# Performance work log

Hardware: AMD Instinct MI355X
Metric: run time of the kernel (lower is better)

Reference implementation:

```python
import jax, jax.numpy as jnp
import numpy as np

EMBED_DIM = 256
CPB_HIDDEN = 256
NUM_HEADS = 8
HEAD_DIM = EMBED_DIM // NUM_HEADS


def setup_inputs() -> dict:
    key = jax.random.key(0)
    ks = jax.random.split(key, 16)
    B, Q, K, D = 2, 256, 2048, EMBED_DIM
    s = 0.02
    return {
        "entities": jax.random.normal(ks[0], (B, Q, D), jnp.float32),
        "images": jax.random.normal(ks[1], (B, K, D), jnp.float32),
        "relative_distances": jax.random.normal(ks[2], (B, Q, K, 2), jnp.float32),
        "Wq": jax.random.normal(ks[3], (D, D), jnp.float32) * s,
        "bq": jnp.zeros((D,), jnp.float32),
        "Wkv": jax.random.normal(ks[4], (2 * D, D), jnp.float32) * s,
        "bkv": jnp.zeros((2 * D,), jnp.float32),
        "W1": jax.random.normal(ks[5], (CPB_HIDDEN, 2), jnp.float32) * s,
        "b1": jnp.zeros((CPB_HIDDEN,), jnp.float32),
        "W2": jax.random.normal(ks[6], (NUM_HEADS, CPB_HIDDEN), jnp.float32) * s,
        "b2": jnp.zeros((NUM_HEADS,), jnp.float32),
        "Wo": jax.random.normal(ks[7], (D, D), jnp.float32) * s,
        "bo": jnp.zeros((D,), jnp.float32),
    }


def reference(entities, images, relative_distances, Wq, bq, Wkv, bkv, W1, b1, W2, b2, Wo, bo):
    B, Q, D = entities.shape
    K = images.shape[1]
    H, hd = NUM_HEADS, HEAD_DIM
    # projections
    q = (entities @ Wq.T + bq).reshape(B, Q, H, hd).transpose(0, 2, 1, 3)  # B H Q hd
    kv = (images @ Wkv.T + bkv).reshape(B, K, 2, H, hd)
    k = kv[:, :, 0].transpose(0, 2, 1, 3)  # B H K hd
    v = kv[:, :, 1].transpose(0, 2, 1, 3)  # B H K hd
    # attention logits
    logits = jnp.einsum("bhqd,bhkd->bhqk", q, k) * (hd ** -0.5)
    # continuous position bias MLP: 2 -> hidden -> num_heads
    h = jax.nn.relu(relative_distances @ W1.T + b1)  # B Q K hidden
    cpb = h @ W2.T + b2  # B Q K H
    logits = logits + cpb.transpose(0, 3, 1, 2)
    attn = jax.nn.softmax(logits, axis=-1)
    out = jnp.einsum("bhqk,bhkd->bhqd", attn, v)
    out = out.transpose(0, 2, 1, 3).reshape(B, Q, D)
    return out @ Wo.T + bo
```

## Files before the change

kernel.cpp:

```cpp
#include <hip/hip_runtime.h>
#include <hip/hip_bf16.h>
#include <cstdint>
#include <cstddef>

#define B_  2
#define Q_  256
#define KL  2048
#define D_  256
#define H_  8
#define HD_ 32
#define CH_ 256

typedef _Float16 f16;
typedef __fp16 fp16x2 __attribute__((ext_vector_type(2)));
typedef _Float16 f16x8 __attribute__((ext_vector_type(8)));
typedef unsigned short ushortv4 __attribute__((ext_vector_type(4)));
typedef unsigned int uintv4 __attribute__((ext_vector_type(4)));
typedef float f32x4 __attribute__((ext_vector_type(4)));

union UH  { fp16x2 h; unsigned int u; };
union UH8 { f16x8 h; unsigned int u[4]; };

__device__ __forceinline__ unsigned int pkrtz(float a, float b) {
  UH r; r.h = __builtin_amdgcn_cvt_pkrtz(a, b); return r.u;
}
__device__ __forceinline__ unsigned short f16bits(float a) {
  return (unsigned short)(pkrtz(a, 0.f) & 0xffffu);
}
__device__ __forceinline__ unsigned int pk_fma(unsigned int a, unsigned int b,
                                               unsigned int c) {
  unsigned int d;
  asm("v_pk_fma_f16 %0, %1, %2, %3" : "=v"(d) : "v"(a), "v"(b), "v"(c));
  return d;
}
__device__ __forceinline__ unsigned int pk_max0(unsigned int a) {
  unsigned int d;
  asm("v_pk_max_f16 %0, %1, %2" : "=v"(d) : "v"(a), "v"(0u));
  return d;
}

__global__ __launch_bounds__(512) void prep(
    const float* __restrict__ ent, const float* __restrict__ img,
    const float* __restrict__ Wq, const float* __restrict__ Wkv,
    const float* __restrict__ Wo,
    unsigned short* __restrict__ entS, unsigned short* __restrict__ imgS,
    unsigned short* __restrict__ WqS, unsigned short* __restrict__ WkvS,
    unsigned short* __restrict__ WoS) {
  int bid = blockIdx.x, t = threadIdx.x;
  const float* src;
  unsigned short* dst;
  if (bid < 32)       { src = ent + (size_t)bid * 16 * D_;          dst = entS + (size_t)bid * 4096; }
  else if (bid < 288) { int k = bid - 32;  src = img + (size_t)k * 16 * D_; dst = imgS + (size_t)k * 4096; }
  else if (bid < 304) { int k = bid - 288; src = Wq  + (size_t)k * 16 * D_; dst = WqS  + (size_t)k * 4096; }
  else if (bid < 336) { int k = bid - 304; src = Wkv + (size_t)k * 16 * D_; dst = WkvS + (size_t)k * 4096; }
  else                { int k = bid - 336; src = Wo  + (size_t)k * 16 * D_; dst = WoS  + (size_t)k * 4096; }
  __shared__ float rows[16][257];
  {
    int rr = t >> 5, c0 = (t & 31) * 8;
    float4 a = *(const float4*)(src + rr * D_ + c0);
    float4 b = *(const float4*)(src + rr * D_ + c0 + 4);
    rows[rr][c0 + 0] = a.x; rows[rr][c0 + 1] = a.y;
    rows[rr][c0 + 2] = a.z; rows[rr][c0 + 3] = a.w;
    rows[rr][c0 + 4] = b.x; rows[rr][c0 + 5] = b.y;
    rows[rr][c0 + 6] = b.z; rows[rr][c0 + 7] = b.w;
  }
  __syncthreads();
  int s = t >> 6, l = t & 63, r = l & 15, g = l >> 4;
  const float* rp = &rows[r][s * 32 + g * 8];
  UH8 u;
#pragma unroll
  for (int m = 0; m < 4; ++m) u.u[m] = pkrtz(rp[2 * m], rp[2 * m + 1]);
  ((f16x8*)dst)[s * 64 + l] = u.h;
}

__global__ __launch_bounds__(256) void gemm2(
    const unsigned short* __restrict__ entS, const unsigned short* __restrict__ WqS,
    const float* __restrict__ bq, float* __restrict__ qp,
    const unsigned short* __restrict__ imgS, const unsigned short* __restrict__ WkvS,
    const float* __restrict__ bkv, unsigned short* __restrict__ kps,
    unsigned short* __restrict__ vt) {
  int bid = blockIdx.x;
  int t = threadIdx.x, w = t >> 6, l = t & 63;
  int r = l & 15, g = l >> 4;
  if (bid < 64) {
    int nt = bid & 3, mg = bid >> 2;
    const f16x8* A = (const f16x8*)entS;
    const f16x8* Bf = (const f16x8*)WqS;
    int tA0 = mg * 2, tB = nt * 4 + w;
    f16x8 a0[8], a1[8], bf[8];
#pragma unroll
    for (int s = 0; s < 8; ++s) {
      a0[s] = A[(tA0 * 8 + s) * 64 + l];
      a1[s] = A[((tA0 + 1) * 8 + s) * 64 + l];
      bf[s] = Bf[(tB * 8 + s) * 64 + l];
    }
    f32x4 acc0 = {0.f, 0.f, 0.f, 0.f}, acc1 = {0.f, 0.f, 0.f, 0.f};
#pragma unroll
    for (int s = 0; s < 8; ++s) {
      acc0 = __builtin_amdgcn_mfma_f32_16x16x32_f16(a0[s], bf[s], acc0, 0, 0, 0);
      acc1 = __builtin_amdgcn_mfma_f32_16x16x32_f16(a1[s], bf[s], acc1, 0, 0, 0);
    }
    int n = nt * 64 + w * 16 + r;
    float bb = bq[n];
    int m0 = mg * 32;
#pragma unroll
    for (int rr = 0; rr < 4; ++rr) {
      qp[(size_t)(m0 + g * 4 + rr) * D_ + n] = acc0[rr] + bb;
      qp[(size_t)(m0 + 16 + g * 4 + rr) * D_ + n] = acc1[rr] + bb;
    }
  } else {
    int bid2 = bid - 64;
    int nt = bid2 & 7, mg = (bid2 >> 3) & 63, b = bid2 >> 9;
    const f16x8* A = (const f16x8*)imgS;
    const f16x8* Bf = (const f16x8*)WkvS;
    int tA0 = b * 128 + mg * 2, tB = nt * 4 + w;
    f16x8 a0[8], a1[8], bf[8];
#pragma unroll
    for (int s = 0; s < 8; ++s) {
      a0[s] = A[(tA0 * 8 + s) * 64 + l];
      a1[s] = A[((tA0 + 1) * 8 + s) * 64 + l];
      bf[s] = Bf[(tB * 8 + s) * 64 + l];
    }
    f32x4 acc0 = {0.f, 0.f, 0.f, 0.f}, acc1 = {0.f, 0.f, 0.f, 0.f};
#pragma unroll
    for (int s = 0; s < 8; ++s) {
      acc0 = __builtin_amdgcn_mfma_f32_16x16x32_f16(a0[s], bf[s], acc0, 0, 0, 0);
      acc1 = __builtin_amdgcn_mfma_f32_16x16x32_f16(a1[s], bf[s], acc1, 0, 0, 0);
    }
    int n = nt * 64 + w * 16 + r;
    float bb = bkv[n];
#pragma unroll
    for (int mi = 0; mi < 2; ++mi) {
      f32x4 ac = (mi == 0) ? acc0 : acc1;
      int mt = mg * 2 + mi;
      if (n < 256) {
        int s2 = n >> 5, gg = (n >> 3) & 3, e = n & 7;
        size_t base = ((size_t)((b * 128 + mt) * 8 + s2) * 64 + gg * 16) * 8 + e;
#pragma unroll
        for (int rr = 0; rr < 4; ++rr)
          kps[base + (size_t)(g * 4 + rr) * 8] = f16bits(ac[rr] + bb);
      } else {
        int c = n - 256, h = c >> 5, dd = c & 31;
        ushortv4 p;
#pragma unroll
        for (int rr = 0; rr < 4; ++rr) p[rr] = f16bits(ac[rr] + bb);
        *(ushortv4*)(vt + ((size_t)(b * H_ + h) * HD_ + dd) * KL + mt * 16 + g * 4) = p;
      }
    }
  }
}

__global__ __launch_bounds__(256, 8) void logits_cpb(
    const float* __restrict__ qp, const unsigned short* __restrict__ kps,
    const float* __restrict__ rd, const float* __restrict__ W1,
    const float* __restrict__ b1, const float* __restrict__ W2,
    const float* __restrict__ b2, unsigned short* __restrict__ lgb,
    float* __restrict__ stats) {
  int gid = blockIdx.x;
  int kcg = gid & 15, qg = (gid >> 4) & 127, b = gid >> 11;
  int t = threadIdx.x;
  __shared__ unsigned int w1xs[128], w1ys[128], b1ps[128];
  __shared__ unsigned short w2h[H_][264];
  __shared__ unsigned int qs[2][128];
  __shared__ float b2s[H_];
  if (t < 128) {
    float4 wr = *(const float4*)(W1 + 4 * t);
    w1xs[t] = pkrtz(wr.x, wr.z);
    w1ys[t] = pkrtz(wr.y, wr.w);
    float2 bb = *(const float2*)(b1 + 2 * t);
    b1ps[t] = pkrtz(bb.x, bb.y);
  }
#pragma unroll
  for (int i = 0; i < 2; ++i) {
    int idx = t + i * 256;
    int h = idx >> 6, c0 = (idx & 63) * 4;
    float4 wv = *(const float4*)(W2 + h * CH_ + c0);
    w2h[h][c0 + 0] = f16bits(wv.x);
    w2h[h][c0 + 1] = f16bits(wv.y);
    w2h[h][c0 + 2] = f16bits(wv.z);
    w2h[h][c0 + 3] = f16bits(wv.w);
  }
  const float scale = 0.17677669529663687f;
  {
    int q = t >> 7, j = t & 127;
    float2 v = *(const float2*)(qp + ((size_t)(b * Q_ + qg * 2 + q) * D_) + 2 * j);
    qs[q][j] = pkrtz(v.x * scale, v.y * scale);
  }
  if (t < 8) b2s[t] = b2[t];
  __syncthreads();

  int l = t & 63, w = t >> 6;
  int hp = l & 15, g = l >> 4, hq = hp & 7;
  int k0 = kcg * 128 + w * 32;
  int kt0 = k0 >> 4;
  int cc = kcg * 4 + w;

  unsigned int x2[2][2], y2[2][2];
#pragma unroll
  for (int q = 0; q < 2; ++q) {
    const float* rdb = rd + ((size_t)(b * Q_ + qg * 2 + q) * KL) * 2;
#pragma unroll
    for (int r = 0; r < 2; ++r) {
      float2 p = *(const float2*)(rdb + (k0 + r * 16 + hp) * 2);
      x2[q][r] = pkrtz(p.x, p.x);
      y2[q][r] = pkrtz(p.y, p.y);
    }
  }

  f32x4 acc[2][2];
#pragma unroll
  for (int q = 0; q < 2; ++q)
#pragma unroll
    for (int r = 0; r < 2; ++r) acc[q][r] = (f32x4){0.f, 0.f, 0.f, 0.f};

  const f16x8* kb = (const f16x8*)kps + ((size_t)(b * 128 + kt0) * 8) * 64 + l;

#pragma unroll
  for (int s = 0; s < 8; ++s) {
    f16x8 kf[2];
#pragma unroll
    for (int r = 0; r < 2; ++r) kf[r] = kb[(r * 8 + s) * 64];
    int pidx = g * 4 + 16 * s;
    uintv4 wx = *(const uintv4*)&w1xs[pidx];
    uintv4 wy = *(const uintv4*)&w1ys[pidx];
    uintv4 bp = *(const uintv4*)&b1ps[pidx];
    f16x8 w2f = *(const f16x8*)&w2h[hq][g * 8 + 32 * s];
    bool sel = (hp == s);
#pragma unroll
    for (int q = 0; q < 2; ++q) {
      uintv4 qv = *(const uintv4*)&qs[q][s * 16 + g * 4];
      UH8 bq;
#pragma unroll
      for (int m = 0; m < 4; ++m) bq.u[m] = sel ? qv[m] : 0u;
#pragma unroll
      for (int r = 0; r < 2; ++r) {
        UH8 az;
#pragma unroll
        for (int m = 0; m < 4; ++m)
          az.u[m] = pk_max0(pk_fma(x2[q][r], wx[m], pk_fma(y2[q][r], wy[m], bp[m])));
        acc[q][r] = __builtin_amdgcn_mfma_f32_16x16x32_f16(az.h, w2f, acc[q][r], 0, 0, 0);
        acc[q][r] = __builtin_amdgcn_mfma_f32_16x16x32_f16(kf[r], bq.h, acc[q][r], 0, 0, 0);
      }
    }
  }

  float bhv = b2s[hq];
#pragma unroll
  for (int q = 0; q < 2; ++q) {
    int qrow = qg * 2 + q;
    float mx = -3.0e38f;
#pragma unroll
    for (int r = 0; r < 2; ++r)
#pragma unroll
      for (int rr = 0; rr < 4; ++rr) {
        acc[q][r][rr] += bhv;
        mx = fmaxf(mx, acc[q][r][rr]);
      }
    mx = fmaxf(mx, __shfl_xor(mx, 16));
    mx = fmaxf(mx, __shfl_xor(mx, 32));
    float ss = 0.f;
#pragma unroll
    for (int r = 0; r < 2; ++r)
#pragma unroll
      for (int rr = 0; rr < 4; ++rr) ss += __expf(acc[q][r][rr] - mx);
    ss += __shfl_xor(ss, 16);
    ss += __shfl_xor(ss, 32);
    if (l < 8)
      *(float2*)(stats + (((size_t)(b * H_ + l) * Q_ + qrow) * 64 + cc) * 2) =
          make_float2(mx, ss);
    if (hp < 8) {
      unsigned short* ob = lgb + ((size_t)(b * H_ + hp) * Q_ + qrow) * KL + k0;
#pragma unroll
      for (int r = 0; r < 2; ++r) {
        uint2 pk;
        pk.x = pkrtz(acc[q][r][0], acc[q][r][1]);
        pk.y = pkrtz(acc[q][r][2], acc[q][r][3]);
        *(uint2*)(ob + r * 16 + g * 4) = pk;
      }
    }
  }
}

__global__ __launch_bounds__(512) void sm_pv(const unsigned short* __restrict__ lgb,
                                             const float* __restrict__ stats,
                                             const unsigned short* __restrict__ vt,
                                             unsigned short* __restrict__ ctxb) {
  int gid = blockIdx.x;
  int qt = gid & 15, bh = gid >> 4;
  int t = threadIdx.x;
  __shared__ float Ms[16], Ss[16];
  __shared__ float pacc[8][16][33];

  {
    int row = t >> 5, cc = t & 31;
    const float2* sp = (const float2*)stats + ((size_t)bh * Q_ + qt * 16 + row) * 64;
    float2 s0 = sp[cc], s1 = sp[cc + 32];
    float m = fmaxf(s0.x, s1.x);
#pragma unroll
    for (int off = 16; off > 0; off >>= 1) m = fmaxf(m, __shfl_xor(m, off));
    float e = s0.y * __expf(s0.x - m) + s1.y * __expf(s1.x - m);
#pragma unroll
    for (int off = 16; off > 0; off >>= 1) e += __shfl_xor(e, off);
    if (cc == 0) { Ms[row] = m; Ss[row] = 1.0f / e; }
  }
  __syncthreads();

  int l = t & 63, w = t >> 6;
  int qq = l & 15, g = l >> 4;
  float mq = Ms[qq];
  const unsigned short* lr2 =
      lgb + ((size_t)bh * Q_ + qt * 16 + qq) * KL + w * 256 + g * 8;
  const unsigned short* vb0 =
      vt + ((size_t)bh * HD_ + qq) * KL + w * 256 + g * 8;
  const unsigned short* vb1 = vb0 + (size_t)16 * KL;
  f32x4 a0 = {0.f, 0.f, 0.f, 0.f}, a1 = {0.f, 0.f, 0.f, 0.f};
#pragma unroll
  for (int step = 0; step < 8; ++step) {
    f16x8 raw = *(const f16x8*)(lr2 + step * 32);
    UH8 pa;
#pragma unroll
    for (int mI = 0; mI < 4; ++mI) {
      float p0 = __expf((float)raw[2 * mI] - mq);
      float p1 = __expf((float)raw[2 * mI + 1] - mq);
      pa.u[mI] = pkrtz(p0, p1);
    }
    f16x8 v0 = *(const f16x8*)(vb0 + step * 32);
    f16x8 v1 = *(const f16x8*)(vb1 + step * 32);
    a0 = __builtin_amdgcn_mfma_f32_16x16x32_f16(pa.h, v0, a0, 0, 0, 0);
    a1 = __builtin_amdgcn_mfma_f32_16x16x32_f16(pa.h, v1, a1, 0, 0, 0);
  }
#pragma unroll
  for (int rr = 0; rr < 4; ++rr) {
    pacc[w][g * 4 + rr][qq] = a0[rr];
    pacc[w][g * 4 + rr][qq + 16] = a1[rr];
  }
  __syncthreads();

  {
    int qo = t >> 5, dd = t & 31;
    float sum = 0.f;
#pragma unroll
    for (int wv = 0; wv < 8; ++wv) sum += pacc[wv][qo][dd];
    sum *= Ss[qo];
    int b = bh >> 3, h = bh & 7;
    ctxb[((size_t)b * Q_ + qt * 16 + qo) * D_ + h * HD_ + dd] = f16bits(sum);
  }
}

__global__ __launch_bounds__(256) void gemm_o(const unsigned short* __restrict__ A,
                                              const unsigned short* __restrict__ WoS,
                                              const float* __restrict__ bias,
                                              float* __restrict__ out) {
  int nt = blockIdx.x & 3, mt = blockIdx.x >> 2;
  int t = threadIdx.x, w = t >> 6, l = t & 63;
  int m0 = mt * 16;
  int r = l & 15, g = l >> 4;
  const unsigned short* arow = A + (size_t)(m0 + r) * D_;
  int tB = nt * 4 + w;
  f16x8 af[8], bf[8];
#pragma unroll
  for (int s = 0; s < 8; ++s) {
    af[s] = *(const f16x8*)(arow + s * 32 + g * 8);
    bf[s] = ((const f16x8*)WoS)[(tB * 8 + s) * 64 + l];
  }
  f32x4 acc = {0.f, 0.f, 0.f, 0.f};
#pragma unroll
  for (int s = 0; s < 8; ++s)
    acc = __builtin_amdgcn_mfma_f32_16x16x32_f16(af[s], bf[s], acc, 0, 0, 0);
  int n = nt * 64 + w * 16 + r;
  float bb = bias[n];
#pragma unroll
  for (int rr = 0; rr < 4; ++rr)
    out[(size_t)(m0 + g * 4 + rr) * D_ + n] = acc[rr] + bb;
}

extern "C" void kernel_launch(void* const* d_in, const int* in_sizes, int n_in,
                              void* d_out, int out_size, void* d_ws, size_t ws_size,
                              hipStream_t stream) {
  const float* ent  = (const float*)d_in[0];
  const float* img  = (const float*)d_in[1];
  const float* rd   = (const float*)d_in[2];
  const float* Wq   = (const float*)d_in[3];
  const float* bq   = (const float*)d_in[4];
  const float* Wkv  = (const float*)d_in[5];
  const float* bkv  = (const float*)d_in[6];
  const float* W1   = (const float*)d_in[7];
  const float* b1   = (const float*)d_in[8];
  const float* W2   = (const float*)d_in[9];
  const float* b2   = (const float*)d_in[10];
  const float* Wo   = (const float*)d_in[11];
  const float* bo   = (const float*)d_in[12];
  float* out = (float*)d_out;

  char* ws = (char*)d_ws;
  float*          qp    = (float*)(ws + 0);
  unsigned short* kps   = (unsigned short*)(ws + 524288);
  unsigned short* vt    = (unsigned short*)(ws + 2621440);
  unsigned short* lgb   = (unsigned short*)(ws + 4718592);
  float*          stats = (float*)(ws + 21495808);
  unsigned short* ctxb  = (unsigned short*)(ws + 23592960);
  unsigned short* entS  = (unsigned short*)(ws + 23855104);
  unsigned short* imgS  = (unsigned short*)(ws + 24117248);
  unsigned short* WqS   = (unsigned short*)(ws + 26214400);
  unsigned short* WkvS  = (unsigned short*)(ws + 26345472);
  unsigned short* WoS   = (unsigned short*)(ws + 26607616);

  prep<<<dim3(352), dim3(512), 0, stream>>>(ent, img, Wq, Wkv, Wo,
                                            entS, imgS, WqS, WkvS, WoS);
  gemm2<<<dim3(64 + 1024), dim3(256), 0, stream>>>(entS, WqS, bq, qp,
                                                   imgS, WkvS, bkv, kps, vt);
  logits_cpb<<<dim3(B_ * 128 * 16), dim3(256), 0, stream>>>(qp, kps, rd, W1, b1, W2, b2, lgb, stats);
  sm_pv<<<dim3(B_ * H_ * 16), dim3(512), 0, stream>>>(lgb, stats, vt, ctxb);
  gemm_o<<<dim3(128), dim3(256), 0, stream>>>(ctxb, WoS, bo, out);
}
```

Measured before the change: 60.59 us.

## Store locally-normalized exp in logits kernel, rescale with packed multiply in PV

The logits kernel now writes exp(logit - chunk_max) in fp16 instead of raw logits. The PV kernel then rescales each 32-key chunk by exp(chunk_max - global_max), using a packed fp16 multiply, rather than recomputing eight exps per step. It also preloads all K fragments up front and relaxes launch bounds from 8 to 4 waves per SIMD to make room for the extra registers. This moves the exp work into the producer and removes it from the consumer's inner loop, at the cost of higher register pressure and lower occupancy.

After: 61.33 us. Within noise of the previous version (+1.2%).

```diff
diff --git a/kernel.cpp b/kernel.cpp
--- a/kernel.cpp
+++ b/kernel.cpp
@@ -36,6 +36,11 @@
 __device__ __forceinline__ unsigned int pk_max0(unsigned int a) {
   unsigned int d;
   asm("v_pk_max_f16 %0, %1, %2" : "=v"(d) : "v"(a), "v"(0u));
+  return d;
+}
+__device__ __forceinline__ unsigned int pk_mul(unsigned int a, unsigned int b) {
+  unsigned int d;
+  asm("v_pk_mul_f16 %0, %1, %2" : "=v"(d) : "v"(a), "v"(b));
   return d;
 }
 
@@ -150,7 +155,7 @@
   }
 }
 
-__global__ __launch_bounds__(256, 8) void logits_cpb(
+__global__ __launch_bounds__(256, 4) void logits_cpb(
     const float* __restrict__ qp, const unsigned short* __restrict__ kps,
     const float* __restrict__ rd, const float* __restrict__ W1,
     const float* __restrict__ b1, const float* __restrict__ W2,
@@ -195,6 +200,13 @@
   int kt0 = k0 >> 4;
   int cc = kcg * 4 + w;
 
+  const f16x8* kb = (const f16x8*)kps + ((size_t)(b * 128 + kt0) * 8) * 64 + l;
+  f16x8 kf[2][8];
+#pragma unroll
+  for (int r = 0; r < 2; ++r)
+#pragma unroll
+    for (int s = 0; s < 8; ++s) kf[r][s] = kb[(r * 8 + s) * 64];
+
   unsigned int x2[2][2], y2[2][2];
 #pragma unroll
   for (int q = 0; q < 2; ++q) {
@@ -213,13 +225,8 @@
 #pragma unroll
     for (int r = 0; r < 2; ++r) acc[q][r] = (f32x4){0.f, 0.f, 0.f, 0.f};
 
-  const f16x8* kb = (const f16x8*)kps + ((size_t)(b * 128 + kt0) * 8) * 64 + l;
-
 #pragma unroll
   for (int s = 0; s < 8; ++s) {
-    f16x8 kf[2];
-#pragma unroll
-    for (int r = 0; r < 2; ++r) kf[r] = kb[(r * 8 + s) * 64];
     int pidx = g * 4 + 16 * s;
     uintv4 wx = *(const uintv4*)&w1xs[pidx];
     uintv4 wy = *(const uintv4*)&w1ys[pidx];
@@ -239,7 +246,7 @@
         for (int m = 0; m < 4; ++m)
           az.u[m] = pk_max0(pk_fma(x2[q][r], wx[m], pk_fma(y2[q][r], wy[m], bp[m])));
         acc[q][r] = __builtin_amdgcn_mfma_f32_16x16x32_f16(az.h, w2f, acc[q][r], 0, 0, 0);
-        acc[q][r] = __builtin_amdgcn_mfma_f32_16x16x32_f16(kf[r], bq.h, acc[q][r], 0, 0, 0);
+        acc[q][r] = __builtin_amdgcn_mfma_f32_16x16x32_f16(kf[r][s], bq.h, acc[q][r], 0, 0, 0);
       }
     }
   }
@@ -258,11 +265,15 @@
       }
     mx = fmaxf(mx, __shfl_xor(mx, 16));
     mx = fmaxf(mx, __shfl_xor(mx, 32));
+    float ex[2][4];
     float ss = 0.f;
 #pragma unroll
     for (int r = 0; r < 2; ++r)
 #pragma unroll
-      for (int rr = 0; rr < 4; ++rr) ss += __expf(acc[q][r][rr] - mx);
+      for (int rr = 0; rr < 4; ++rr) {
+        ex[r][rr] = __expf(acc[q][r][rr] - mx);
+        ss += ex[r][rr];
+      }
     ss += __shfl_xor(ss, 16);
     ss += __shfl_xor(ss, 32);
     if (l < 8)
@@ -273,8 +284,8 @@
 #pragma unroll
       for (int r = 0; r < 2; ++r) {
         uint2 pk;
-        pk.x = pkrtz(acc[q][r][0], acc[q][r][1]);
-        pk.y = pkrtz(acc[q][r][2], acc[q][r][3]);
+        pk.x = pkrtz(ex[r][0], ex[r][1]);
+        pk.y = pkrtz(ex[r][2], ex[r][3]);
         *(uint2*)(ob + r * 16 + g * 4) = pk;
       }
     }
@@ -288,7 +299,8 @@
   int gid = blockIdx.x;
   int qt = gid & 15, bh = gid >> 4;
   int t = threadIdx.x;
-  __shared__ float Ms[16], Ss[16];
+  __shared__ float Ss[16];
+  __shared__ float scl[16][65];
   __shared__ float pacc[8][16][33];
 
   {
@@ -298,16 +310,18 @@
     float m = fmaxf(s0.x, s1.x);
 #pragma unroll
     for (int off = 16; off > 0; off >>= 1) m = fmaxf(m, __shfl_xor(m, off));
-    float e = s0.y * __expf(s0.x - m) + s1.y * __expf(s1.x - m);
+    float c0 = __expf(s0.x - m), c1 = __expf(s1.x - m);
+    float e = s0.y * c0 + s1.y * c1;
 #pragma unroll
     for (int off = 16; off > 0; off >>= 1) e += __shfl_xor(e, off);
-    if (cc == 0) { Ms[row] = m; Ss[row] = 1.0f / e; }
+    scl[row][cc] = c0;
+    scl[row][cc + 32] = c1;
+    if (cc == 0) Ss[row] = 1.0f / e;
   }
   __syncthreads();
 
   int l = t & 63, w = t >> 6;
   int qq = l & 15, g = l >> 4;
-  float mq = Ms[qq];
   const unsigned short* lr2 =
       lgb + ((size_t)bh * Q_ + qt * 16 + qq) * KL + w * 256 + g * 8;
   const unsigned short* vb0 =
@@ -316,14 +330,12 @@
   f32x4 a0 = {0.f, 0.f, 0.f, 0.f}, a1 = {0.f, 0.f, 0.f, 0.f};
 #pragma unroll
   for (int step = 0; step < 8; ++step) {
-    f16x8 raw = *(const f16x8*)(lr2 + step * 32);
+    UH8 raw = *(const UH8*)(lr2 + step * 32);
+    float sc = scl[qq][w * 8 + step];
+    unsigned int sc2 = pkrtz(sc, sc);
     UH8 pa;
 #pragma unroll
-    for (int mI = 0; mI < 4; ++mI) {
-      float p0 = __expf((float)raw[2 * mI] - mq);
-      float p1 = __expf((float)raw[2 * mI + 1] - mq);
-      pa.u[mI] = pkrtz(p0, p1);
-    }
+    for (int mI = 0; mI < 4; ++mI) pa.u[mI] = pk_mul(raw.u[mI], sc2);
     f16x8 v0 = *(const f16x8*)(vb0 + step * 32);
     f16x8 v1 = *(const f16x8*)(vb1 + step * 32);
     a0 = __builtin_amdgcn_mfma_f32_16x16x32_f16(pa.h, v0, a0, 0, 0, 0);
```

## Move QK logits into attention kernel and make CPB kernel bias-only

Applied to the files above, without the earlier changes.

The CPB kernel now produces only the position-bias MLP output, in an MFMA-accumulator-friendly fp16 layout. The attention kernel computes Q·K with the bias loaded as the accumulator, then does a full-row softmax in registers with cross-wave LDS reductions before the PV matmul. This removes the partial max/sum stats buffer and the extra MFMAs in the CPB kernel. The scaled Q is pre-written in fp16 fragment layout by the projection GEMM. The trade-off is more per-block work in the low-occupancy attention kernel, and the per-head b2 bias is dropped, relying on softmax shift invariance.

After: 54.80 us. -9.5%, faster.

```diff
diff --git a/kernel.cpp b/kernel.cpp
--- a/kernel.cpp
+++ b/kernel.cpp
@@ -26,6 +26,10 @@
 }
 __device__ __forceinline__ unsigned short f16bits(float a) {
   return (unsigned short)(pkrtz(a, 0.f) & 0xffffu);
+}
+__device__ __forceinline__ float h2f(unsigned short u) {
+  __fp16 h = *(__fp16*)&u;
+  return (float)h;
 }
 __device__ __forceinline__ unsigned int pk_fma(unsigned int a, unsigned int b,
                                                unsigned int c) {
@@ -75,13 +79,14 @@
 
 __global__ __launch_bounds__(256) void gemm2(
     const unsigned short* __restrict__ entS, const unsigned short* __restrict__ WqS,
-    const float* __restrict__ bq, float* __restrict__ qp,
+    const float* __restrict__ bq, unsigned short* __restrict__ qpf,
     const unsigned short* __restrict__ imgS, const unsigned short* __restrict__ WkvS,
     const float* __restrict__ bkv, unsigned short* __restrict__ kps,
     unsigned short* __restrict__ vt) {
   int bid = blockIdx.x;
   int t = threadIdx.x, w = t >> 6, l = t & 63;
   int r = l & 15, g = l >> 4;
+  const float scale = 0.17677669529663687f;
   if (bid < 64) {
     int nt = bid & 3, mg = bid >> 2;
     const f16x8* A = (const f16x8*)entS;
@@ -102,11 +107,18 @@
     }
     int n = nt * 64 + w * 16 + r;
     float bb = bq[n];
+    int h = n >> 5, gq = (n >> 3) & 3, e = n & 7;
     int m0 = mg * 32;
 #pragma unroll
-    for (int rr = 0; rr < 4; ++rr) {
-      qp[(size_t)(m0 + g * 4 + rr) * D_ + n] = acc0[rr] + bb;
-      qp[(size_t)(m0 + 16 + g * 4 + rr) * D_ + n] = acc1[rr] + bb;
+    for (int half = 0; half < 2; ++half) {
+      f32x4 ac = half ? acc1 : acc0;
+#pragma unroll
+      for (int rr = 0; rr < 4; ++rr) {
+        int row = m0 + half * 16 + g * 4 + rr;
+        int qt_g = row >> 4, rq = row & 15;
+        qpf[((size_t)(qt_g * 8 + h)) * 512 + (gq * 16 + rq) * 8 + e] =
+            f16bits((ac[rr] + bb) * scale);
+      }
     }
   } else {
     int bid2 = bid - 64;
@@ -150,19 +162,15 @@
   }
 }
 
-__global__ __launch_bounds__(256, 8) void logits_cpb(
-    const float* __restrict__ qp, const unsigned short* __restrict__ kps,
+__global__ __launch_bounds__(256, 8) void cpb_k(
     const float* __restrict__ rd, const float* __restrict__ W1,
     const float* __restrict__ b1, const float* __restrict__ W2,
-    const float* __restrict__ b2, unsigned short* __restrict__ lgb,
-    float* __restrict__ stats) {
+    unsigned short* __restrict__ cpb4) {
   int gid = blockIdx.x;
   int kcg = gid & 15, qg = (gid >> 4) & 127, b = gid >> 11;
   int t = threadIdx.x;
   __shared__ unsigned int w1xs[128], w1ys[128], b1ps[128];
   __shared__ unsigned short w2h[H_][264];
-  __shared__ unsigned int qs[2][128];
-  __shared__ float b2s[H_];
   if (t < 128) {
     float4 wr = *(const float4*)(W1 + 4 * t);
     w1xs[t] = pkrtz(wr.x, wr.z);
@@ -180,20 +188,12 @@
     w2h[h][c0 + 2] = f16bits(wv.z);
     w2h[h][c0 + 3] = f16bits(wv.w);
   }
-  const float scale = 0.17677669529663687f;
-  {
-    int q = t >> 7, j = t & 127;
-    float2 v = *(const float2*)(qp + ((size_t)(b * Q_ + qg * 2 + q) * D_) + 2 * j);
-    qs[q][j] = pkrtz(v.x * scale, v.y * scale);
-  }
-  if (t < 8) b2s[t] = b2[t];
   __syncthreads();
 
   int l = t & 63, w = t >> 6;
   int hp = l & 15, g = l >> 4, hq = hp & 7;
   int k0 = kcg * 128 + w * 32;
   int kt0 = k0 >> 4;
-  int cc = kcg * 4 + w;
 
   unsigned int x2[2][2], y2[2][2];
 #pragma unroll
@@ -213,25 +213,15 @@
 #pragma unroll
     for (int r = 0; r < 2; ++r) acc[q][r] = (f32x4){0.f, 0.f, 0.f, 0.f};
 
-  const f16x8* kb = (const f16x8*)kps + ((size_t)(b * 128 + kt0) * 8) * 64 + l;
-
 #pragma unroll
   for (int s = 0; s < 8; ++s) {
-    f16x8 kf[2];
-#pragma unroll
-    for (int r = 0; r < 2; ++r) kf[r] = kb[(r * 8 + s) * 64];
     int pidx = g * 4 + 16 * s;
     uintv4 wx = *(const uintv4*)&w1xs[pidx];
     uintv4 wy = *(const uintv4*)&w1ys[pidx];
     uintv4 bp = *(const uintv4*)&b1ps[pidx];
     f16x8 w2f = *(const f16x8*)&w2h[hq][g * 8 + 32 * s];
-    bool sel = (hp == s);
-#pragma unroll
-    for (int q = 0; q < 2; ++q) {
-      uintv4 qv = *(const uintv4*)&qs[q][s * 16 + g * 4];
-      UH8 bq;
-#pragma unroll
-      for (int m = 0; m < 4; ++m) bq.u[m] = sel ? qv[m] : 0u;
+#pragma unroll
+    for (int q = 0; q < 2; ++q)
 #pragma unroll
       for (int r = 0; r < 2; ++r) {
         UH8 az;
@@ -239,95 +229,106 @@
         for (int m = 0; m < 4; ++m)
           az.u[m] = pk_max0(pk_fma(x2[q][r], wx[m], pk_fma(y2[q][r], wy[m], bp[m])));
         acc[q][r] = __builtin_amdgcn_mfma_f32_16x16x32_f16(az.h, w2f, acc[q][r], 0, 0, 0);
-        acc[q][r] = __builtin_amdgcn_mfma_f32_16x16x32_f16(kf[r], bq.h, acc[q][r], 0, 0, 0);
       }
-    }
-  }
-
-  float bhv = b2s[hq];
-#pragma unroll
-  for (int q = 0; q < 2; ++q) {
-    int qrow = qg * 2 + q;
-    float mx = -3.0e38f;
-#pragma unroll
-    for (int r = 0; r < 2; ++r)
-#pragma unroll
-      for (int rr = 0; rr < 4; ++rr) {
-        acc[q][r][rr] += bhv;
-        mx = fmaxf(mx, acc[q][r][rr]);
-      }
-    mx = fmaxf(mx, __shfl_xor(mx, 16));
-    mx = fmaxf(mx, __shfl_xor(mx, 32));
-    float ss = 0.f;
-#pragma unroll
-    for (int r = 0; r < 2; ++r)
-#pragma unroll
-      for (int rr = 0; rr < 4; ++rr) ss += __expf(acc[q][r][rr] - mx);
-    ss += __shfl_xor(ss, 16);
-    ss += __shfl_xor(ss, 32);
-    if (l < 8)
-      *(float2*)(stats + (((size_t)(b * H_ + l) * Q_ + qrow) * 64 + cc) * 2) =
-          make_float2(mx, ss);
-    if (hp < 8) {
-      unsigned short* ob = lgb + ((size_t)(b * H_ + hp) * Q_ + qrow) * KL + k0;
+  }
+
+  if (hp < 8) {
+#pragma unroll
+    for (int q = 0; q < 2; ++q) {
+      int qrow = qg * 2 + q;
+      int qt = qrow >> 4, qc = qrow & 15;
 #pragma unroll
       for (int r = 0; r < 2; ++r) {
+        size_t T = ((size_t)(b * 8 + hp) * 128 + kt0 + r) * 16 + qt;
         uint2 pk;
         pk.x = pkrtz(acc[q][r][0], acc[q][r][1]);
         pk.y = pkrtz(acc[q][r][2], acc[q][r][3]);
-        *(uint2*)(ob + r * 16 + g * 4) = pk;
+        *(uint2*)(cpb4 + T * 256 + (g * 16 + qc) * 4) = pk;
       }
     }
   }
 }
 
-__global__ __launch_bounds__(512) void sm_pv(const unsigned short* __restrict__ lgb,
-                                             const float* __restrict__ stats,
-                                             const unsigned short* __restrict__ vt,
-                                             unsigned short* __restrict__ ctxb) {
+__global__ __launch_bounds__(512) void attn(
+    const unsigned short* __restrict__ qpf, const unsigned short* __restrict__ kps,
+    const unsigned short* __restrict__ cpb4, const unsigned short* __restrict__ vt,
+    unsigned short* __restrict__ ctxb) {
   int gid = blockIdx.x;
   int qt = gid & 15, bh = gid >> 4;
-  int t = threadIdx.x;
-  __shared__ float Ms[16], Ss[16];
+  int b = bh >> 3, h = bh & 7;
+  int t = threadIdx.x, w = t >> 6, l = t & 63;
+  int qq = l & 15, g = l >> 4;
+  __shared__ unsigned short Plds[8][16][256];
+  __shared__ float wred[8][16];
   __shared__ float pacc[8][16][33];
 
+  UH8 qB;
   {
-    int row = t >> 5, cc = t & 31;
-    const float2* sp = (const float2*)stats + ((size_t)bh * Q_ + qt * 16 + row) * 64;
-    float2 s0 = sp[cc], s1 = sp[cc + 32];
-    float m = fmaxf(s0.x, s1.x);
-#pragma unroll
-    for (int off = 16; off > 0; off >>= 1) m = fmaxf(m, __shfl_xor(m, off));
-    float e = s0.y * __expf(s0.x - m) + s1.y * __expf(s1.x - m);
-#pragma unroll
-    for (int off = 16; off > 0; off >>= 1) e += __shfl_xor(e, off);
-    if (cc == 0) { Ms[row] = m; Ss[row] = 1.0f / e; }
-  }
+    const unsigned int* qpu = (const unsigned int*)qpf;
+    uintv4 qv = *(const uintv4*)(qpu + ((size_t)((b * 16 + qt) * 8 + h)) * 256 + l * 4);
+#pragma unroll
+    for (int m = 0; m < 4; ++m) qB.u[m] = qv[m];
+  }
+
+  const f16x8* ka = (const f16x8*)kps + ((size_t)(b * 128) * 8) * 64 + l;
+  const unsigned short* cb = cpb4 + ((size_t)bh * 128 * 16 + qt) * 256 + l * 4;
+  f32x4 S[16];
+#pragma unroll
+  for (int i = 0; i < 16; ++i) {
+    int kt = w * 16 + i;
+    uint2 c2 = *(const uint2*)(cb + (size_t)kt * 4096);
+    f32x4 C;
+    C[0] = h2f((unsigned short)(c2.x & 0xffff));
+    C[1] = h2f((unsigned short)(c2.x >> 16));
+    C[2] = h2f((unsigned short)(c2.y & 0xffff));
+    C[3] = h2f((unsigned short)(c2.y >> 16));
+    f16x8 af = ka[((size_t)kt * 8 + h) * 64];
+    S[i] = __builtin_amdgcn_mfma_f32_16x16x32_f16(af, qB.h, C, 0, 0, 0);
+  }
+
+  float m = -3.0e38f;
+#pragma unroll
+  for (int i = 0; i < 16; ++i)
+#pragma unroll
+    for (int rr = 0; rr < 4; ++rr) m = fmaxf(m, S[i][rr]);
+  m = fmaxf(m, __shfl_xor(m, 16));
+  m = fmaxf(m, __shfl_xor(m, 32));
+  if (l < 16) wred[w][l] = m;
   __syncthreads();
-
-  int l = t & 63, w = t >> 6;
-  int qq = l & 15, g = l >> 4;
-  float mq = Ms[qq];
-  const unsigned short* lr2 =
-      lgb + ((size_t)bh * Q_ + qt * 16 + qq) * KL + w * 256 + g * 8;
-  const unsigned short* vb0 =
-      vt + ((size_t)bh * HD_ + qq) * KL + w * 256 + g * 8;
+  float M = wred[0][qq];
+#pragma unroll
+  for (int wv = 1; wv < 8; ++wv) M = fmaxf(M, wred[wv][qq]);
+  __syncthreads();
+
+  float ss = 0.f;
+  char* prow = (char*)&Plds[w][qq][0];
+  int xr = (qq & 7) << 4;
+#pragma unroll
+  for (int i = 0; i < 16; ++i) {
+    float p0 = __expf(S[i][0] - M);
+    float p1 = __expf(S[i][1] - M);
+    float p2 = __expf(S[i][2] - M);
+    float p3 = __expf(S[i][3] - M);
+    ss += (p0 + p1) + (p2 + p3);
+    uint2 pk;
+    pk.x = pkrtz(p0, p1);
+    pk.y = pkrtz(p2, p3);
+    *(uint2*)(prow + ((i * 32 + g * 8) ^ xr)) = pk;
+  }
+  ss += __shfl_xor(ss, 16);
+  ss += __shfl_xor(ss, 32);
+  if (l < 16) wred[w][l] = ss;
+
+  const unsigned short* vb0 = vt + ((size_t)bh * HD_ + qq) * KL + w * 256 + g * 8;
   const unsigned short* vb1 = vb0 + (size_t)16 * KL;
   f32x4 a0 = {0.f, 0.f, 0.f, 0.f}, a1 = {0.f, 0.f, 0.f, 0.f};
 #pragma unroll
-  for (int step = 0; step < 8; ++step) {
-    f16x8 raw = *(const f16x8*)(lr2 + step * 32);
-    UH8 pa;
-#pragma unroll
-    for (int mI = 0; mI < 4; ++mI) {
-      float p0 = __expf((float)raw[2 * mI] - mq);
-      float p1 = __expf((float)raw[2 * mI + 1] - mq);
-      pa.u[mI] = pkrtz(p0, p1);
-    }
-    f16x8 v0 = *(const f16x8*)(vb0 + step * 32);
-    f16x8 v1 = *(const f16x8*)(vb1 + step * 32);
-    a0 = __builtin_amdgcn_mfma_f32_16x16x32_f16(pa.h, v0, a0, 0, 0, 0);
-    a1 = __builtin_amdgcn_mfma_f32_16x16x32_f16(pa.h, v1, a1, 0, 0, 0);
+  for (int cw = 0; cw < 8; ++cw) {
+    f16x8 pa = *(const f16x8*)(prow + ((cw * 64 + g * 16) ^ xr));
+    f16x8 v0 = *(const f16x8*)(vb0 + cw * 32);
+    f16x8 v1 = *(const f16x8*)(vb1 + cw * 32);
+    a0 = __builtin_amdgcn_mfma_f32_16x16x32_f16(pa, v0, a0, 0, 0, 0);
+    a1 = __builtin_amdgcn_mfma_f32_16x16x32_f16(pa, v1, a1, 0, 0, 0);
   }
 #pragma unroll
   for (int rr = 0; rr < 4; ++rr) {
@@ -338,12 +339,13 @@
 
   {
     int qo = t >> 5, dd = t & 31;
-    float sum = 0.f;
-#pragma unroll
-    for (int wv = 0; wv < 8; ++wv) sum += pacc[wv][qo][dd];
-    sum *= Ss[qo];
-    int b = bh >> 3, h = bh & 7;
-    ctxb[((size_t)b * Q_ + qt * 16 + qo) * D_ + h * HD_ + dd] = f16bits(sum);
+    float sum = 0.f, st = 0.f;
+#pragma unroll
+    for (int wv = 0; wv < 8; ++wv) {
+      sum += pacc[wv][qo][dd];
+      st += wred[wv][qo];
+    }
+    ctxb[((size_t)b * Q_ + qt * 16 + qo) * D_ + h * HD_ + dd] = f16bits(sum / st);
   }
 }
 
@@ -391,25 +393,25 @@
   const float* Wo   = (const float*)d_in[11];
   const float* bo   = (const float*)d_in[12];
   float* out = (float*)d_out;
+  (void)b2;
 
   char* ws = (char*)d_ws;
-  float*          qp    = (float*)(ws + 0);
-  unsigned short* kps   = (unsigned short*)(ws + 524288);
-  unsigned short* vt    = (unsigned short*)(ws + 2621440);
-  unsigned short* lgb   = (unsigned short*)(ws + 4718592);
-  float*          stats = (float*)(ws + 21495808);
-  unsigned short* ctxb  = (unsigned short*)(ws + 23592960);
-  unsigned short* entS  = (unsigned short*)(ws + 23855104);
-  unsigned short* imgS  = (unsigned short*)(ws + 24117248);
-  unsigned short* WqS   = (unsigned short*)(ws + 26214400);
-  unsigned short* WkvS  = (unsigned short*)(ws + 26345472);
-  unsigned short* WoS   = (unsigned short*)(ws + 26607616);
+  unsigned short* kps   = (unsigned short*)(ws + 0);
+  unsigned short* vt    = (unsigned short*)(ws + 2097152);
+  unsigned short* cpb4  = (unsigned short*)(ws + 4194304);
+  unsigned short* ctxb  = (unsigned short*)(ws + 20971520);
+  unsigned short* qpf   = (unsigned short*)(ws + 21233664);
+  unsigned short* entS  = (unsigned short*)(ws + 21495808);
+  unsigned short* imgS  = (unsigned short*)(ws + 21757952);
+  unsigned short* WqS   = (unsigned short*)(ws + 23855104);
+  unsigned short* WkvS  = (unsigned short*)(ws + 23986176);
+  unsigned short* WoS   = (unsigned short*)(ws + 24248320);
 
   prep<<<dim3(352), dim3(512), 0, stream>>>(ent, img, Wq, Wkv, Wo,
                                             entS, imgS, WqS, WkvS, WoS);
-  gemm2<<<dim3(64 + 1024), dim3(256), 0, stream>>>(entS, WqS, bq, qp,
+  gemm2<<<dim3(64 + 1024), dim3(256), 0, stream>>>(entS, WqS, bq, qpf,
                                                    imgS, WkvS, bkv, kps, vt);
-  logits_cpb<<<dim3(B_ * 128 * 16), dim3(256), 0, stream>>>(qp, kps, rd, W1, b1, W2, b2, lgb, stats);
-  sm_pv<<<dim3(B_ * H_ * 16), dim3(512), 0, stream>>>(lgb, stats, vt, ctxb);
+  cpb_k<<<dim3(B_ * 128 * 16), dim3(256), 0, stream>>>(rd, W1, b1, W2, cpb4);
+  attn<<<dim3(B_ * H_ * 16), dim3(512), 0, stream>>>(qpf, kps, cpb4, vt, ctxb);
   gemm_o<<<dim3(128), dim3(256), 0, stream>>>(ctxb, WoS, bo, out);
 }
```
